# Performance work log

Measured on AMD Instinct MI355X. Metric: run time of the kernel, lower is better.

Reference implementation:

```python
import jax, jax.numpy as jnp
import numpy as np
from jax import lax

TEMPERATURE = 30.0
BN_EPS = 1e-5


def setup_inputs() -> dict:
    key = jax.random.key(0)
    ks = jax.random.split(key, 9)
    B, H, W, C_in = 32, 64, 64, 128
    n_filters, r_filters, n_kernels = 128, 4, 4
    x = jax.random.normal(ks[0], (B, H, W, C_in), dtype=jnp.float32)
    reduction_kernel = jax.random.normal(ks[1], (C_in, r_filters), dtype=jnp.float32) * 0.02
    attention_kernel = jax.random.normal(ks[2], (r_filters, n_kernels), dtype=jnp.float32) * 0.02
    conv_kernels = jax.random.normal(ks[3], (n_kernels, 3, 3, C_in, n_filters), dtype=jnp.float32) * 0.05
    bias = jax.random.normal(ks[4], (n_kernels, n_filters), dtype=jnp.float32) * 0.05
    bn_scale = jax.random.uniform(ks[5], (n_filters,), dtype=jnp.float32, minval=0.5, maxval=1.5)
    bn_bias = jax.random.normal(ks[6], (n_filters,), dtype=jnp.float32) * 0.1
    bn_mean = jax.random.normal(ks[7], (n_filters,), dtype=jnp.float32) * 0.1
    bn_var = jax.random.uniform(ks[8], (n_filters,), dtype=jnp.float32, minval=0.5, maxval=1.5)
    return {"x": x, "reduction_kernel": reduction_kernel, "attention_kernel": attention_kernel,
            "conv_kernels": conv_kernels, "bias": bias, "bn_scale": bn_scale, "bn_bias": bn_bias,
            "bn_mean": bn_mean, "bn_var": bn_var}


def reference(x, reduction_kernel, attention_kernel, conv_kernels, bias, bn_scale, bn_bias, bn_mean, bn_var):
    # x: [B,H,W,C_in] NHWC. Inference mode (training=False): BN uses running stats.
    B = x.shape[0]
    # Squeeze-style routing: global average pool -> reduce -> relu -> attention over experts.
    pool = jnp.mean(x, axis=(1, 2))                             # [B, C_in]
    pool_red = jax.nn.relu(pool @ reduction_kernel)             # [B, r]
    attention = jax.nn.softmax((pool_red @ attention_kernel) / TEMPERATURE, axis=-1)  # [B, K]
    # Soft mixture of conv expert kernels, per sample.
    w_mixed = jnp.einsum('bk,khwio->bhwio', attention, conv_kernels)  # [B,kH,kW,C_in,F]

    def per_sample_conv(xi, wi):
        # xi: [H,W,C_in], wi: [kH,kW,C_in,F]
        return lax.conv_general_dilated(xi[None], wi, window_strides=(1, 1), padding='SAME',
                                        dimension_numbers=('NHWC', 'HWIO', 'NHWC'))[0]

    y = jax.vmap(per_sample_conv)(x, w_mixed)                   # [B,H,W,F]
    b_mixed = attention @ bias                                  # [B, F]
    y = y + b_mixed[:, None, None, :]
    # BatchNorm (inference) + relu
    inv = bn_scale * lax.rsqrt(bn_var + BN_EPS)
    y = (y - bn_mean) * inv + bn_bias
    return jax.nn.relu(y)
```

## Files before the change

kernel.cpp:

```cpp
#include <hip/hip_runtime.h>

typedef short bf16x8 __attribute__((ext_vector_type(8)));
typedef float f32x4 __attribute__((ext_vector_type(4)));
typedef unsigned int u32x4 __attribute__((ext_vector_type(4)));
typedef unsigned short u16x4 __attribute__((ext_vector_type(4)));

__device__ __forceinline__ unsigned short f2bf(float f) {
  unsigned u = __builtin_bit_cast(unsigned, f);
  u = (u + 0x7FFFu + ((u >> 16) & 1u)) >> 16;
  return (unsigned short)u;
}

__global__ __launch_bounds__(256) void k_pool_cvt(const float* __restrict__ x,
                                                  unsigned short* __restrict__ xb,
                                                  float* __restrict__ pp) {
  const int slice = blockIdx.x;
  const int b = blockIdx.y;
  const int t = threadIdx.x;
  const int c4 = (t & 31) * 4;
  const int seg = t >> 5;
  const size_t base = ((size_t)b * 4096 + slice * 256 + seg * 32) * 128;
  const float* xp = x + base;
  unsigned short* xbp = xb + base;
  f32x4 s = {0.f, 0.f, 0.f, 0.f};
  for (int p = 0; p < 32; ++p) {
    f32x4 v = *(const f32x4*)(xp + p * 128 + c4);
    s += v;
    u16x4 h;
    h.x = f2bf(v.x); h.y = f2bf(v.y); h.z = f2bf(v.z); h.w = f2bf(v.w);
    *(u16x4*)(xbp + p * 128 + c4) = h;
  }
  __shared__ f32x4 red[256];
  red[t] = s;
  __syncthreads();
  if (t < 32) {
    f32x4 tot = red[t];
#pragma unroll
    for (int g = 1; g < 8; ++g) tot += red[g * 32 + t];
    *(f32x4*)(pp + (size_t)(b * 16 + slice) * 128 + t * 4) = tot;
  }
}

__global__ __launch_bounds__(128) void k_route(const float* __restrict__ pp,
    const float* __restrict__ redk, const float* __restrict__ attk,
    const float* __restrict__ bias, const float* __restrict__ bns,
    const float* __restrict__ bnb, const float* __restrict__ bnm,
    const float* __restrict__ bnv,
    float* __restrict__ att_ws, float* __restrict__ beta_ws,
    float* __restrict__ alpha_ws) {
  const int b = blockIdx.x, t = threadIdx.x;
  __shared__ float pool[128];
  __shared__ float att[4];
  {
    float s = 0.f;
    for (int i = 0; i < 16; ++i) s += pp[(size_t)(b * 16 + i) * 128 + t];
    pool[t] = s * (1.f / 4096.f);
  }
  __syncthreads();
  if (t == 0) {
    float pr[4];
    for (int r = 0; r < 4; ++r) {
      float s = 0.f;
      for (int c = 0; c < 128; ++c) s += pool[c] * redk[c * 4 + r];
      pr[r] = fmaxf(s, 0.f);
    }
    float lgt[4]; float mx = -1e30f;
    for (int k = 0; k < 4; ++k) {
      float s = 0.f;
      for (int r = 0; r < 4; ++r) s += pr[r] * attk[r * 4 + k];
      lgt[k] = s * (1.f / 30.f);
      mx = fmaxf(mx, lgt[k]);
    }
    float den = 0.f;
    for (int k = 0; k < 4; ++k) { lgt[k] = expf(lgt[k] - mx); den += lgt[k]; }
    for (int k = 0; k < 4; ++k) { att[k] = lgt[k] / den; att_ws[b * 4 + k] = att[k]; }
  }
  __syncthreads();
  {
    float bm = 0.f;
    for (int k = 0; k < 4; ++k) bm += att[k] * bias[k * 128 + t];
    const float inv = bns[t] * rsqrtf(bnv[t] + 1e-5f);
    beta_ws[b * 128 + t] = (bm - bnm[t]) * inv + bnb[t];
    alpha_ws[t] = inv;
  }
}

__global__ __launch_bounds__(256) void k_mixw(const float* __restrict__ ck,
                                              const float* __restrict__ att_ws,
                                              unsigned short* __restrict__ w_ws) {
  const int bx = blockIdx.x;
  const int tap = bx >> 4;
  const int cq = (bx >> 2) & 3;
  const int fq = bx & 3;
  const int t = threadIdx.x;
  __shared__ float cw[4][32][32];
  __shared__ float attl[128];
  if (t < 128) attl[t] = att_ws[t];
  {
    const int k = t >> 6, c = (t & 63) >> 1, f0 = (t & 1) * 16;
    const float* src = ck + ((size_t)(k * 9 + tap) * 128 + cq * 32 + c) * 128
                          + fq * 32 + f0;
    *(f32x4*)&cw[k][c][f0]      = *(const f32x4*)(src);
    *(f32x4*)&cw[k][c][f0 + 4]  = *(const f32x4*)(src + 4);
    *(f32x4*)&cw[k][c][f0 + 8]  = *(const f32x4*)(src + 8);
    *(f32x4*)&cw[k][c][f0 + 12] = *(const f32x4*)(src + 12);
  }
  __syncthreads();
  const int f = t & 31, o = (t >> 5) & 3, sh = t >> 7;
  const int fp = fq * 32 + f;
  const int h = cq >> 1;
  const int oslab = (cq & 1) * 4 + o;
  const int chunk = fp * 8 + (oslab ^ (fp & 7));
  float wv[4][8];
#pragma unroll
  for (int k = 0; k < 4; ++k)
#pragma unroll
    for (int j = 0; j < 8; ++j) wv[k][j] = cw[k][o * 8 + j][f];
#pragma unroll
  for (int bs = 0; bs < 16; ++bs) {
    const int b = sh * 16 + bs;
    const float a0 = attl[b * 4 + 0], a1 = attl[b * 4 + 1];
    const float a2 = attl[b * 4 + 2], a3 = attl[b * 4 + 3];
    bf16x8 ov;
#pragma unroll
    for (int j = 0; j < 8; ++j) {
      const float v = a0 * wv[0][j] + a1 * wv[1][j] + a2 * wv[2][j] + a3 * wv[3][j];
      ov[j] = (short)f2bf(v);
    }
    *(bf16x8*)(w_ws + (size_t)b * 147456 + (size_t)(h * 9 + tap) * 8192
               + (size_t)chunk * 8) = ov;
  }
}

__device__ __forceinline__ void stage_w16(char* dst, const unsigned short* src, int t) {
#pragma unroll
  for (int j = 0; j < 2; ++j) {
    const int i = t + j * 512;
    __builtin_amdgcn_global_load_lds(
        (const __attribute__((address_space(1))) void*)(src + (size_t)i * 8),
        (__attribute__((address_space(3))) void*)(dst + i * 16), 16, 0, 0);
  }
}

__device__ __forceinline__ void stage_x_half(char* xt, const unsigned short* xbp,
                                             int r0, int h, int t) {
  const int pix = t >> 3;
  const int oct = (t & 7) ^ ((t >> 3) & 7);
#pragma unroll
  for (int j = 0; j < 6; ++j) {
    const int rr = r0 - 1 + j;
    char* dst = xt + j * 8192 + t * 16;
    if ((unsigned)rr < 64u) {
      __builtin_amdgcn_global_load_lds(
          (const __attribute__((address_space(1))) void*)
              (xbp + ((size_t)(rr * 64 + pix)) * 128 + h * 64 + oct * 8),
          (__attribute__((address_space(3))) void*)dst, 16, 0, 0);
    } else {
      *(u32x4*)dst = (u32x4){0, 0, 0, 0};
    }
  }
}

__global__ __launch_bounds__(512, 4) void k_conv(const unsigned short* __restrict__ xb,
                                                 const unsigned short* __restrict__ w_ws,
                                                 const float* __restrict__ alpha_ws,
                                                 const float* __restrict__ beta_ws,
                                                 float* __restrict__ out) {
  extern __shared__ char lds[];
  char* xt = lds;
  char* wlds = lds + 49152;

  const int orig = blockIdx.x;
  const int wg = (orig & 7) * 64 + (orig >> 3);
  const int b = wg >> 4;
  const int tile = wg & 15;
  const int t = threadIdx.x;
  const int lane = t & 63, wid = t >> 6;
  const int wm = wid >> 1, wn = wid & 1;
  const int lr = lane & 15, lg = lane >> 4;
  const int r0 = tile * 4;

  const unsigned short* xbp = xb + (size_t)b * 4096 * 128;
  const unsigned short* wsrc = w_ws + (size_t)b * 18 * 8192;

  f32x4 acc[4][4] = {};
  const bf16x8 zero = {};

  stage_x_half(xt, xbp, r0, 0, t);
  stage_w16(wlds, wsrc, t);
  asm volatile("s_waitcnt vmcnt(0) lgkmcnt(0)" ::: "memory");
  __builtin_amdgcn_s_barrier();
  asm volatile("" ::: "memory");

  for (int s = 0; s < 18; ++s) {
    const int tap = s % 9;
    char* cb = wlds + ((s & 1) << 14);
    if (s < 17) stage_w16(wlds + (((s + 1) & 1) << 14),
                          wsrc + (size_t)(s + 1) * 8192, t);

    const int dh = tap / 3 - 1, dw = tap % 3 - 1;
    const int jrow = wm + dh + 1;
#pragma unroll
    for (int kc = 0; kc < 2; ++kc) {
      bf16x8 afr[4], bfr[4];
#pragma unroll
      for (int mf = 0; mf < 4; ++mf) {
        const int col = mf * 16 + lr + dw;
        const int a = ((jrow * 64 + col) * 128 + kc * 64 + lg * 16) ^ ((col & 7) << 4);
        afr[mf] = ((unsigned)col < 64u) ? *(const bf16x8*)(xt + a) : zero;
      }
#pragma unroll
      for (int nf = 0; nf < 4; ++nf) {
        const int f = wn * 64 + nf * 16 + lr;
        const int a = (f * 128 + kc * 64 + lg * 16) ^ ((f & 7) << 4);
        bfr[nf] = *(const bf16x8*)(cb + a);
      }
      __builtin_amdgcn_s_setprio(1);
#pragma unroll
      for (int mf = 0; mf < 4; ++mf)
#pragma unroll
        for (int nf = 0; nf < 4; ++nf)
          acc[mf][nf] = __builtin_amdgcn_mfma_f32_16x16x32_bf16(afr[mf], bfr[nf],
                                                                acc[mf][nf], 0, 0, 0);
      __builtin_amdgcn_s_setprio(0);
    }
    asm volatile("" ::: "memory");

    if (s == 8) {
      __builtin_amdgcn_s_barrier();
      stage_x_half(xt, xbp, r0, 1, t);
      asm volatile("s_waitcnt vmcnt(0) lgkmcnt(0)" ::: "memory");
      __builtin_amdgcn_s_barrier();
      asm volatile("" ::: "memory");
    } else if (s < 17) {
      asm volatile("s_waitcnt vmcnt(0)" ::: "memory");
      __builtin_amdgcn_s_barrier();
      asm volatile("" ::: "memory");
    }
  }

  float af[4], bt[4];
#pragma unroll
  for (int nf = 0; nf < 4; ++nf) {
    const int f = wn * 64 + nf * 16 + lr;
    af[nf] = alpha_ws[f];
    bt[nf] = beta_ws[b * 128 + f];
  }
  float* op = out + (size_t)b * 4096 * 128;
  const int row = r0 + wm;
#pragma unroll
  for (int mf = 0; mf < 4; ++mf) {
#pragma unroll
    for (int r = 0; r < 4; ++r) {
      const int col = mf * 16 + lg * 4 + r;
#pragma unroll
      for (int nf = 0; nf < 4; ++nf) {
        const int f = wn * 64 + nf * 16 + lr;
        const float v = acc[mf][nf][r] * af[nf] + bt[nf];
        op[(size_t)(row * 64 + col) * 128 + f] = fmaxf(v, 0.f);
      }
    }
  }
}

extern "C" void kernel_launch(void* const* d_in, const int* in_sizes, int n_in,
                              void* d_out, int out_size, void* d_ws, size_t ws_size,
                              hipStream_t stream) {
  const float* x    = (const float*)d_in[0];
  const float* redk = (const float*)d_in[1];
  const float* attk = (const float*)d_in[2];
  const float* ck   = (const float*)d_in[3];
  const float* bias = (const float*)d_in[4];
  const float* bns  = (const float*)d_in[5];
  const float* bnbb = (const float*)d_in[6];
  const float* bnm  = (const float*)d_in[7];
  const float* bnv  = (const float*)d_in[8];
  float* out = (float*)d_out;

  char* ws = (char*)d_ws;
  unsigned short* xb   = (unsigned short*)ws;
  unsigned short* w_ws = (unsigned short*)(ws + 33554432);
  float* pp       = (float*)(ws + 42991616);
  float* att_ws   = (float*)(ws + 43253760);
  float* beta_ws  = (float*)(ws + 43254272);
  float* alpha_ws = (float*)(ws + 43270656);

  k_pool_cvt<<<dim3(16, 32), 256, 0, stream>>>(x, xb, pp);
  k_route<<<32, 128, 0, stream>>>(pp, redk, attk, bias, bns, bnbb, bnm, bnv,
                                  att_ws, beta_ws, alpha_ws);
  k_mixw<<<144, 256, 0, stream>>>(ck, att_ws, w_ws);
  k_conv<<<512, 512, 81920, stream>>>(xb, w_ws, alpha_ws, beta_ws, out);
}
```

Before: 75.41 us.

## Fuse bf16 conversion of x into conv staging and drop bf16 copy

The pooling kernel no longer writes a bf16 copy of x. The conv kernel instead loads fp32 x directly, converts it to bf16 in registers and stores it swizzled into LDS. This removes the 32MB bf16 write and one pass of traffic. In exchange, the conv loses async global-to-LDS loads for x and reads twice as many bytes per element with halo overlap. Fragment loads for both k-chunks are now hoisted before the MFMA block, at the cost of more live registers.

```diff
diff --git a/kernel.cpp b/kernel.cpp
--- a/kernel.cpp
+++ b/kernel.cpp
@@ -11,9 +11,8 @@
   return (unsigned short)u;
 }
 
-__global__ __launch_bounds__(256) void k_pool_cvt(const float* __restrict__ x,
-                                                  unsigned short* __restrict__ xb,
-                                                  float* __restrict__ pp) {
+__global__ __launch_bounds__(256) void k_pool(const float* __restrict__ x,
+                                              float* __restrict__ pp) {
   const int slice = blockIdx.x;
   const int b = blockIdx.y;
   const int t = threadIdx.x;
@@ -21,15 +20,8 @@
   const int seg = t >> 5;
   const size_t base = ((size_t)b * 4096 + slice * 256 + seg * 32) * 128;
   const float* xp = x + base;
-  unsigned short* xbp = xb + base;
   f32x4 s = {0.f, 0.f, 0.f, 0.f};
-  for (int p = 0; p < 32; ++p) {
-    f32x4 v = *(const f32x4*)(xp + p * 128 + c4);
-    s += v;
-    u16x4 h;
-    h.x = f2bf(v.x); h.y = f2bf(v.y); h.z = f2bf(v.z); h.w = f2bf(v.w);
-    *(u16x4*)(xbp + p * 128 + c4) = h;
-  }
+  for (int p = 0; p < 32; ++p) s += *(const f32x4*)(xp + p * 128 + c4);
   __shared__ f32x4 red[256];
   red[t] = s;
   __syncthreads();
@@ -142,26 +134,31 @@
   }
 }
 
-__device__ __forceinline__ void stage_x_half(char* xt, const unsigned short* xbp,
+__device__ __forceinline__ void stage_x_half(char* xt, const float* xp,
                                              int r0, int h, int t) {
   const int pix = t >> 3;
-  const int oct = (t & 7) ^ ((t >> 3) & 7);
+  const int oct = t & 7;
+  const int swz = (pix & 7) << 4;
 #pragma unroll
   for (int j = 0; j < 6; ++j) {
     const int rr = r0 - 1 + j;
-    char* dst = xt + j * 8192 + t * 16;
+    char* dst = xt + ((j * 8192 + t * 16) ^ swz);
     if ((unsigned)rr < 64u) {
-      __builtin_amdgcn_global_load_lds(
-          (const __attribute__((address_space(1))) void*)
-              (xbp + ((size_t)(rr * 64 + pix)) * 128 + h * 64 + oct * 8),
-          (__attribute__((address_space(3))) void*)dst, 16, 0, 0);
+      const float* s = xp + ((size_t)(rr * 64 + pix)) * 128 + h * 64 + oct * 8;
+      f32x4 v0 = *(const f32x4*)s;
+      f32x4 v1 = *(const f32x4*)(s + 4);
+      u16x4 h0, h1;
+      h0.x = f2bf(v0.x); h0.y = f2bf(v0.y); h0.z = f2bf(v0.z); h0.w = f2bf(v0.w);
+      h1.x = f2bf(v1.x); h1.y = f2bf(v1.y); h1.z = f2bf(v1.z); h1.w = f2bf(v1.w);
+      *(u16x4*)dst = h0;
+      *(u16x4*)(dst + 8) = h1;
     } else {
       *(u32x4*)dst = (u32x4){0, 0, 0, 0};
     }
   }
 }
 
-__global__ __launch_bounds__(512, 4) void k_conv(const unsigned short* __restrict__ xb,
+__global__ __launch_bounds__(512, 4) void k_conv(const float* __restrict__ x,
                                                  const unsigned short* __restrict__ w_ws,
                                                  const float* __restrict__ alpha_ws,
                                                  const float* __restrict__ beta_ws,
@@ -180,13 +177,13 @@
   const int lr = lane & 15, lg = lane >> 4;
   const int r0 = tile * 4;
 
-  const unsigned short* xbp = xb + (size_t)b * 4096 * 128;
+  const float* xp = x + (size_t)b * 4096 * 128;
   const unsigned short* wsrc = w_ws + (size_t)b * 18 * 8192;
 
   f32x4 acc[4][4] = {};
   const bf16x8 zero = {};
 
-  stage_x_half(xt, xbp, r0, 0, t);
+  stage_x_half(xt, xp, r0, 0, t);
   stage_w16(wlds, wsrc, t);
   asm volatile("s_waitcnt vmcnt(0) lgkmcnt(0)" ::: "memory");
   __builtin_amdgcn_s_barrier();
@@ -200,35 +197,38 @@
 
     const int dh = tap / 3 - 1, dw = tap % 3 - 1;
     const int jrow = wm + dh + 1;
+    bf16x8 afr[2][4], bfr[2][4];
 #pragma unroll
     for (int kc = 0; kc < 2; ++kc) {
-      bf16x8 afr[4], bfr[4];
+      const int kx = kc << 6;
 #pragma unroll
       for (int mf = 0; mf < 4; ++mf) {
         const int col = mf * 16 + lr + dw;
-        const int a = ((jrow * 64 + col) * 128 + kc * 64 + lg * 16) ^ ((col & 7) << 4);
-        afr[mf] = ((unsigned)col < 64u) ? *(const bf16x8*)(xt + a) : zero;
+        const int a = (((jrow * 64 + col) * 128 + lg * 16) ^ ((col & 7) << 4)) ^ kx;
+        afr[kc][mf] = ((unsigned)col < 64u) ? *(const bf16x8*)(xt + a) : zero;
       }
 #pragma unroll
       for (int nf = 0; nf < 4; ++nf) {
         const int f = wn * 64 + nf * 16 + lr;
-        const int a = (f * 128 + kc * 64 + lg * 16) ^ ((f & 7) << 4);
-        bfr[nf] = *(const bf16x8*)(cb + a);
+        const int a = ((f * 128 + lg * 16) ^ ((f & 7) << 4)) ^ kx;
+        bfr[kc][nf] = *(const bf16x8*)(cb + a);
       }
-      __builtin_amdgcn_s_setprio(1);
+    }
+    __builtin_amdgcn_s_setprio(1);
+#pragma unroll
+    for (int kc = 0; kc < 2; ++kc)
 #pragma unroll
       for (int mf = 0; mf < 4; ++mf)
 #pragma unroll
         for (int nf = 0; nf < 4; ++nf)
-          acc[mf][nf] = __builtin_amdgcn_mfma_f32_16x16x32_bf16(afr[mf], bfr[nf],
-                                                                acc[mf][nf], 0, 0, 0);
-      __builtin_amdgcn_s_setprio(0);
-    }
+          acc[mf][nf] = __builtin_amdgcn_mfma_f32_16x16x32_bf16(
+              afr[kc][mf], bfr[kc][nf], acc[mf][nf], 0, 0, 0);
+    __builtin_amdgcn_s_setprio(0);
     asm volatile("" ::: "memory");
 
     if (s == 8) {
       __builtin_amdgcn_s_barrier();
-      stage_x_half(xt, xbp, r0, 1, t);
+      stage_x_half(xt, xp, r0, 1, t);
       asm volatile("s_waitcnt vmcnt(0) lgkmcnt(0)" ::: "memory");
       __builtin_amdgcn_s_barrier();
       asm volatile("" ::: "memory");
@@ -278,16 +278,15 @@
   float* out = (float*)d_out;
 
   char* ws = (char*)d_ws;
-  unsigned short* xb   = (unsigned short*)ws;
   unsigned short* w_ws = (unsigned short*)(ws + 33554432);
   float* pp       = (float*)(ws + 42991616);
   float* att_ws   = (float*)(ws + 43253760);
   float* beta_ws  = (float*)(ws + 43254272);
   float* alpha_ws = (float*)(ws + 43270656);
 
-  k_pool_cvt<<<dim3(16, 32), 256, 0, stream>>>(x, xb, pp);
+  k_pool<<<dim3(16, 32), 256, 0, stream>>>(x, pp);
   k_route<<<32, 128, 0, stream>>>(pp, redk, attk, bias, bns, bnbb, bnm, bnv,
                                   att_ws, beta_ws, alpha_ws);
   k_mixw<<<144, 256, 0, stream>>>(ck, att_ws, w_ws);
-  k_conv<<<512, 512, 81920, stream>>>(xb, w_ws, alpha_ws, beta_ws, out);
-}
+  k_conv<<<512, 512, 81920, stream>>>(x, w_ws, alpha_ws, beta_ws, out);
+}
```

Result: slower. 112.9 us (+49.7%).

## Split conv tap loop into barrier-synced phases with partial vmcnt waits

Applied to the files above, without the earlier changes.

Each tap iteration is rewritten as two macro-expanded K phases. Each phase loads fragments from LDS, hits a workgroup barrier, waits on LDS reads, runs its MFMAs behind a scheduling barrier, and ends with another barrier. The end-of-step full vmcnt(0) wait is replaced by a vmcnt(2) wait at the start of the next step. This is meant to keep the next tap's weight prefetch in flight while the current tap's MFMAs run, and to interleave waves in lockstep. In exchange it adds more barriers per iteration. The LDS weight reads may now run before other threads' async copies are made visible by a barrier.

```diff
diff --git a/kernel.cpp b/kernel.cpp
--- a/kernel.cpp
+++ b/kernel.cpp
@@ -161,6 +161,37 @@
   }
 }
 
+#define PHASE(KC)                                                              \
+  {                                                                            \
+    bf16x8 afr[4], bfr[4];                                                     \
+    _Pragma("unroll")                                                          \
+    for (int mf = 0; mf < 4; ++mf) {                                           \
+      const int col = mf * 16 + lr + dw;                                       \
+      const int a = ((jrow * 64 + col) * 128 + (KC) * 64 + lg * 16)            \
+                    ^ ((col & 7) << 4);                                        \
+      afr[mf] = ((unsigned)col < 64u) ? *(const bf16x8*)(xt + a) : zero;       \
+    }                                                                          \
+    _Pragma("unroll")                                                          \
+    for (int nf = 0; nf < 4; ++nf) {                                           \
+      const int f = wn * 64 + nf * 16 + lr;                                    \
+      const int a = (f * 128 + (KC) * 64 + lg * 16) ^ ((f & 7) << 4);          \
+      bfr[nf] = *(const bf16x8*)(cb + a);                                      \
+    }                                                                          \
+    __builtin_amdgcn_s_barrier();                                              \
+    asm volatile("s_waitcnt lgkmcnt(0)" ::: "memory");                         \
+    __builtin_amdgcn_sched_barrier(0);                                         \
+    __builtin_amdgcn_s_setprio(1);                                             \
+    _Pragma("unroll")                                                          \
+    for (int mf = 0; mf < 4; ++mf)                                             \
+      _Pragma("unroll")                                                        \
+      for (int nf = 0; nf < 4; ++nf)                                           \
+        acc[mf][nf] = __builtin_amdgcn_mfma_f32_16x16x32_bf16(afr[mf],         \
+                          bfr[nf], acc[mf][nf], 0, 0, 0);                      \
+    __builtin_amdgcn_s_setprio(0);                                             \
+    asm volatile("" ::: "memory");                                             \
+    __builtin_amdgcn_s_barrier();                                              \
+  }
+
 __global__ __launch_bounds__(512, 4) void k_conv(const unsigned short* __restrict__ xb,
                                                  const unsigned short* __restrict__ w_ws,
                                                  const float* __restrict__ alpha_ws,
@@ -195,45 +226,22 @@
   for (int s = 0; s < 18; ++s) {
     const int tap = s % 9;
     char* cb = wlds + ((s & 1) << 14);
+    const int dh = tap / 3 - 1, dw = tap % 3 - 1;
+    const int jrow = wm + dh + 1;
+
     if (s < 17) stage_w16(wlds + (((s + 1) & 1) << 14),
                           wsrc + (size_t)(s + 1) * 8192, t);
-
-    const int dh = tap / 3 - 1, dw = tap % 3 - 1;
-    const int jrow = wm + dh + 1;
-#pragma unroll
-    for (int kc = 0; kc < 2; ++kc) {
-      bf16x8 afr[4], bfr[4];
-#pragma unroll
-      for (int mf = 0; mf < 4; ++mf) {
-        const int col = mf * 16 + lr + dw;
-        const int a = ((jrow * 64 + col) * 128 + kc * 64 + lg * 16) ^ ((col & 7) << 4);
-        afr[mf] = ((unsigned)col < 64u) ? *(const bf16x8*)(xt + a) : zero;
-      }
-#pragma unroll
-      for (int nf = 0; nf < 4; ++nf) {
-        const int f = wn * 64 + nf * 16 + lr;
-        const int a = (f * 128 + kc * 64 + lg * 16) ^ ((f & 7) << 4);
-        bfr[nf] = *(const bf16x8*)(cb + a);
-      }
-      __builtin_amdgcn_s_setprio(1);
-#pragma unroll
-      for (int mf = 0; mf < 4; ++mf)
-#pragma unroll
-        for (int nf = 0; nf < 4; ++nf)
-          acc[mf][nf] = __builtin_amdgcn_mfma_f32_16x16x32_bf16(afr[mf], bfr[nf],
-                                                                acc[mf][nf], 0, 0, 0);
-      __builtin_amdgcn_s_setprio(0);
-    }
-    asm volatile("" ::: "memory");
+    if (s > 0) {
+      if (s < 17) { asm volatile("s_waitcnt vmcnt(2)" ::: "memory"); }
+      else        { asm volatile("s_waitcnt vmcnt(0)" ::: "memory"); }
+    }
+
+    PHASE(0)
+    PHASE(1)
 
     if (s == 8) {
-      __builtin_amdgcn_s_barrier();
       stage_x_half(xt, xbp, r0, 1, t);
       asm volatile("s_waitcnt vmcnt(0) lgkmcnt(0)" ::: "memory");
-      __builtin_amdgcn_s_barrier();
-      asm volatile("" ::: "memory");
-    } else if (s < 17) {
-      asm volatile("s_waitcnt vmcnt(0)" ::: "memory");
       __builtin_amdgcn_s_barrier();
       asm volatile("" ::: "memory");
     }
```

Result: slower. 81.07 us (+7.5%).
